# Kernel tuning notes

Measured on AMD Instinct MI355X. Metric: run time of the kernel, lower is better.

Reference implementation:

```python
import jax, jax.numpy as jnp
import numpy as np

B, D_IN, N_NODES, NNZ = 128, 64, 50000, 800000


def setup_inputs() -> dict:
    key = jax.random.key(0)
    k1, k2, k3, k4, k5 = jax.random.split(key, 5)
    x = jax.random.normal(k1, (B, D_IN), dtype=jnp.float32)
    # weight init ~ uniform(-1/sqrt(out), 1/sqrt(out)) per reset(); scale kept tiny
    stdv = 1.0 / np.sqrt(N_NODES)
    weight = jax.random.uniform(k2, (D_IN, N_NODES), dtype=jnp.float32,
                                minval=-stdv, maxval=stdv)
    adj_rows = jax.random.randint(k3, (NNZ,), 0, N_NODES)
    adj_cols = jax.random.randint(k4, (NNZ,), 0, N_NODES)
    adj_vals = jax.random.normal(k5, (NNZ,), dtype=jnp.float32)
    return {"x": x, "weight": weight, "adj_rows": adj_rows,
            "adj_cols": adj_cols, "adj_vals": adj_vals}


def reference(x, weight, adj_rows, adj_cols, adj_vals):
    # m = x @ W : [B, N]
    m = jnp.dot(x, weight)
    # m @ adj (sparse COO): out[b, c] = sum_e m[b, rows[e]] * vals[e] where cols[e] == c
    gathered = m[:, adj_rows] * adj_vals  # [B, NNZ]
    out = jnp.zeros(m.shape, m.dtype).at[:, adj_cols].add(gathered)
    return out
```

## Files before the change

kernel.cpp:

```cpp
#include <hip/hip_runtime.h>

#define B_    128
#define DIN_  64
#define NN_   50000
#define NNZ_  800000
#define CAP_  64
#define NC_   16

#define GEMM_BLOCKS_   782
#define BUCKET_BLOCKS_ 1563
#define FUSED_BLOCKS_  2345

__device__ __forceinline__ unsigned short f2bf(float f) {
    unsigned int u = __float_as_uint(f);
    u += 0x7FFFu + ((u >> 16) & 1u);
    return (unsigned short)(u >> 16);
}

__global__ __launch_bounds__(512) void fused_gb(const float* __restrict__ x,
                                                const float* __restrict__ W,
                                                unsigned short* __restrict__ m_bf,
                                                const int* __restrict__ rows,
                                                const int* __restrict__ cols,
                                                const float* __restrict__ vals,
                                                int* __restrict__ cnt,
                                                unsigned int* __restrict__ csc) {
    __shared__ float xs_t[DIN_][132];
    const int t = threadIdx.x;
    const int g = blockIdx.x / 3;
    const int r = blockIdx.x % 3;

    if (r != 0) {
        const int bid = 2 * g + (r - 1);
        if (bid >= BUCKET_BLOCKS_) return;
        const int e = bid * 512 + t;
        if (e >= NNZ_) return;
        const int c = cols[e];
        const int pos = atomicAdd(&cnt[c], 1);
        if (pos < CAP_)
            csc[((unsigned int)c << 6) + pos] =
                ((unsigned int)rows[e] << 16) | (unsigned int)f2bf(vals[e]);
        return;
    }

    for (int i = t; i < B_ * DIN_; i += 512)
        xs_t[i & 63][i >> 6] = x[i];
    __syncthreads();

    const int l  = t & 63;
    const int n  = g * 64 + l;
    const int nc = n < NN_ ? n : NN_ - 1;
    const int b0 = (t >> 6) * 16;

    float acc[16];
    #pragma unroll
    for (int j = 0; j < 16; ++j) acc[j] = 0.f;

    const float* Wp = W + nc;
    float wcur[8], wnxt[8];
    #pragma unroll
    for (int q = 0; q < 8; ++q) wcur[q] = Wp[(size_t)q * NN_];

    for (int k = 0; k < DIN_; k += 8) {
        const int kn = k + 8;
        if (kn < DIN_) {
            #pragma unroll
            for (int q = 0; q < 8; ++q) wnxt[q] = Wp[(size_t)(kn + q) * NN_];
        }
        #pragma unroll
        for (int q = 0; q < 8; ++q) {
            const float wv = wcur[q];
            const float4* xp = reinterpret_cast<const float4*>(&xs_t[k + q][b0]);
            const float4 x0 = xp[0], x1 = xp[1], x2 = xp[2], x3 = xp[3];
            acc[0]  += wv * x0.x;  acc[1]  += wv * x0.y;
            acc[2]  += wv * x0.z;  acc[3]  += wv * x0.w;
            acc[4]  += wv * x1.x;  acc[5]  += wv * x1.y;
            acc[6]  += wv * x1.z;  acc[7]  += wv * x1.w;
            acc[8]  += wv * x2.x;  acc[9]  += wv * x2.y;
            acc[10] += wv * x2.z;  acc[11] += wv * x2.w;
            acc[12] += wv * x3.x;  acc[13] += wv * x3.y;
            acc[14] += wv * x3.z;  acc[15] += wv * x3.w;
        }
        #pragma unroll
        for (int q = 0; q < 8; ++q) wcur[q] = wnxt[q];
    }

    if (n < NN_) {
        unsigned int pk[8];
        #pragma unroll
        for (int j = 0; j < 8; ++j)
            pk[j] = (unsigned int)f2bf(acc[2 * j]) |
                    ((unsigned int)f2bf(acc[2 * j + 1]) << 16);
        uint4* op = reinterpret_cast<uint4*>(m_bf + (size_t)n * B_ + b0);
        op[0] = make_uint4(pk[0], pk[1], pk[2], pk[3]);
        op[1] = make_uint4(pk[4], pk[5], pk[6], pk[7]);
    }
}

__global__ __launch_bounds__(256) void gather_k(const unsigned short* __restrict__ m_bf,
                                                const int* __restrict__ cnt,
                                                const unsigned int* __restrict__ csc,
                                                float* __restrict__ out) {
    __shared__ float tile[B_][NC_ + 1];
    const int t    = threadIdx.x;
    const int g    = t >> 6;
    const int lane = t & 63;
    const int c0   = blockIdx.x * NC_;

    #pragma unroll
    for (int cl = 0; cl < 4; ++cl) {
        const int c = c0 + g * 4 + cl;
        const unsigned int* ce = &csc[(unsigned int)c << 6];
        int n = cnt[c]; if (n > CAP_) n = CAP_;

        float acc0 = 0.f, acc1 = 0.f;
        int e = 0;
        for (; e + 7 < n; e += 8) {
            unsigned int p[8], mm[8];
            #pragma unroll
            for (int q = 0; q < 8; ++q) p[q] = ce[e + q];
            #pragma unroll
            for (int q = 0; q < 8; ++q)
                mm[q] = *(const unsigned int*)(m_bf + (((size_t)(p[q] >> 16)) << 7) + (lane << 1));
            #pragma unroll
            for (int q = 0; q < 8; ++q) {
                const float v = __uint_as_float(p[q] << 16);
                acc0 += __uint_as_float(mm[q] << 16)         * v;
                acc1 += __uint_as_float(mm[q] & 0xFFFF0000u) * v;
            }
        }
        for (; e + 3 < n; e += 4) {
            unsigned int p[4], mm[4];
            #pragma unroll
            for (int q = 0; q < 4; ++q) p[q] = ce[e + q];
            #pragma unroll
            for (int q = 0; q < 4; ++q)
                mm[q] = *(const unsigned int*)(m_bf + (((size_t)(p[q] >> 16)) << 7) + (lane << 1));
            #pragma unroll
            for (int q = 0; q < 4; ++q) {
                const float v = __uint_as_float(p[q] << 16);
                acc0 += __uint_as_float(mm[q] << 16)         * v;
                acc1 += __uint_as_float(mm[q] & 0xFFFF0000u) * v;
            }
        }
        for (; e < n; ++e) {
            const unsigned int p = ce[e];
            const unsigned int m = *(const unsigned int*)(m_bf + (((size_t)(p >> 16)) << 7) + (lane << 1));
            const float v = __uint_as_float(p << 16);
            acc0 += __uint_as_float(m << 16)         * v;
            acc1 += __uint_as_float(m & 0xFFFF0000u) * v;
        }
        tile[2 * lane][g * 4 + cl]     = acc0;
        tile[2 * lane + 1][g * 4 + cl] = acc1;
    }
    __syncthreads();

    const int r = t >> 1, h = t & 1;
    const float* tr = &tile[r][h * 8];
    const float4 w0 = make_float4(tr[0], tr[1], tr[2], tr[3]);
    const float4 w1 = make_float4(tr[4], tr[5], tr[6], tr[7]);
    float4* op = reinterpret_cast<float4*>(&out[(size_t)r * NN_ + c0 + h * 8]);
    op[0] = w0;
    op[1] = w1;
}

__global__ __launch_bounds__(256) void scatter_onfly(const float* __restrict__ x,
                                                     const float* __restrict__ W,
                                                     const int* __restrict__ rows,
                                                     const int* __restrict__ cols,
                                                     const float* __restrict__ vals,
                                                     float* __restrict__ out) {
    const unsigned int gid = blockIdx.x * 256u + threadIdx.x;
    const unsigned int e = gid >> 7;
    const unsigned int b = gid & 127u;
    if (e >= NNZ_) return;
    const int   r = rows[e];
    const int   c = cols[e];
    const float v = vals[e];
    float dot = 0.f;
    for (int k = 0; k < DIN_; ++k)
        dot += x[b * DIN_ + k] * W[(size_t)k * NN_ + r];
    atomicAdd(&out[(size_t)b * NN_ + c], dot * v);
}

extern "C" void kernel_launch(void* const* d_in, const int* in_sizes, int n_in,
                              void* d_out, int out_size, void* d_ws, size_t ws_size,
                              hipStream_t stream) {
    const float* x    = (const float*)d_in[0];
    const float* W    = (const float*)d_in[1];
    const int*   rows = (const int*)d_in[2];
    const int*   cols = (const int*)d_in[3];
    const float* vals = (const float*)d_in[4];
    float* out = (float*)d_out;

    const size_t mbf_bytes = (size_t)NN_ * B_ * sizeof(unsigned short);
    const size_t cnt_bytes = (size_t)NN_ * sizeof(int);
    const size_t csc_bytes = (size_t)NN_ * CAP_ * sizeof(unsigned int);
    const size_t need = mbf_bytes + cnt_bytes + csc_bytes;

    const int gather_blocks = NN_ / NC_;

    if (ws_size >= need) {
        char* p = (char*)d_ws;
        unsigned short* m_bf = (unsigned short*)p;  p += mbf_bytes;
        int*            cnt  = (int*)p;             p += cnt_bytes;
        unsigned int*   csc  = (unsigned int*)p;

        hipMemsetAsync(cnt, 0, cnt_bytes, stream);
        fused_gb<<<FUSED_BLOCKS_, 512, 0, stream>>>(x, W, m_bf, rows, cols, vals, cnt, csc);
        gather_k<<<gather_blocks, 256, 0, stream>>>(m_bf, cnt, csc, out);
    } else {
        const int scatter_blocks = (NNZ_ * 128) / 256;
        hipMemsetAsync(out, 0, (size_t)NN_ * B_ * sizeof(float), stream);
        scatter_onfly<<<scatter_blocks, 256, 0, stream>>>(x, W, rows, cols, vals, out);
    }
}
```

Before: 165.6 us.

## Fuse memset, GEMM/bucketing and gather into one cooperative persistent kernel

Replaces the memset plus two-kernel pipeline with a single cooperative kernel. It zeroes the counters, runs GEMM and bucketing on alternating blocks, and performs the gather in grid-stride 32-column tiles, with grid.sync barriers between phases. The aim is to remove launch overhead and the inter-kernel gaps. In exchange it adds two grid-wide barriers and a persistent grid sized by occupancy, which may hide memory latency less well in the latency-bound gather phase. The old multi-kernel path is kept as a fallback if the cooperative launch fails.

```diff
diff --git a/kernel.cpp b/kernel.cpp
--- a/kernel.cpp
+++ b/kernel.cpp
@@ -1,21 +1,173 @@
 #include <hip/hip_runtime.h>
+#include <hip/hip_cooperative_groups.h>
+
+namespace cg = cooperative_groups;
 
 #define B_    128
 #define DIN_  64
 #define NN_   50000
 #define NNZ_  800000
 #define CAP_  64
-#define NC_   16
-
-#define GEMM_BLOCKS_   782
-#define BUCKET_BLOCKS_ 1563
-#define FUSED_BLOCKS_  2345
+
+#define GEMM_TILES_   782
+#define GATHER_TILES_ 1563
 
 __device__ __forceinline__ unsigned short f2bf(float f) {
     unsigned int u = __float_as_uint(f);
     u += 0x7FFFu + ((u >> 16) & 1u);
     return (unsigned short)(u >> 16);
 }
+
+__global__ __launch_bounds__(512) void fused_all(const float* __restrict__ x,
+                                                 const float* __restrict__ W,
+                                                 unsigned short* __restrict__ m_bf,
+                                                 const int* __restrict__ rows,
+                                                 const int* __restrict__ cols,
+                                                 const float* __restrict__ vals,
+                                                 int* __restrict__ cnt,
+                                                 unsigned int* __restrict__ csc,
+                                                 float* __restrict__ out) {
+    __shared__ float smem[DIN_ * 132];
+    cg::grid_group grid = cg::this_grid();
+    const int t   = threadIdx.x;
+    const int blk = blockIdx.x;
+    const int nb  = gridDim.x;
+
+    for (int i = blk * 512 + t; i < NN_; i += nb * 512)
+        cnt[i] = 0;
+    grid.sync();
+
+    if (blk & 1) {
+        const int nbb = nb >> 1;
+        const int idx = blk >> 1;
+        for (int e = idx * 512 + t; e < NNZ_; e += nbb * 512) {
+            const int c = cols[e];
+            const int pos = atomicAdd(&cnt[c], 1);
+            if (pos < CAP_)
+                csc[((unsigned int)c << 6) + pos] =
+                    ((unsigned int)rows[e] << 16) | (unsigned int)f2bf(vals[e]);
+        }
+    } else {
+        float (*xs_t)[132] = reinterpret_cast<float (*)[132]>(smem);
+        for (int i = t; i < B_ * DIN_; i += 512)
+            xs_t[i & 63][i >> 6] = x[i];
+        __syncthreads();
+
+        const int nbg = (nb + 1) >> 1;
+        const int idx = blk >> 1;
+        const int l   = t & 63;
+        const int b0  = (t >> 6) * 16;
+
+        for (int tile = idx; tile < GEMM_TILES_; tile += nbg) {
+            const int n  = tile * 64 + l;
+            const int nc = n < NN_ ? n : NN_ - 1;
+
+            float acc[16];
+            #pragma unroll
+            for (int j = 0; j < 16; ++j) acc[j] = 0.f;
+
+            const float* Wp = W + nc;
+            float wcur[8], wnxt[8];
+            #pragma unroll
+            for (int q = 0; q < 8; ++q) wcur[q] = Wp[(size_t)q * NN_];
+
+            for (int k = 0; k < DIN_; k += 8) {
+                const int kn = k + 8;
+                if (kn < DIN_) {
+                    #pragma unroll
+                    for (int q = 0; q < 8; ++q) wnxt[q] = Wp[(size_t)(kn + q) * NN_];
+                }
+                #pragma unroll
+                for (int q = 0; q < 8; ++q) {
+                    const float wv = wcur[q];
+                    const float4* xp = reinterpret_cast<const float4*>(&xs_t[k + q][b0]);
+                    const float4 x0 = xp[0], x1 = xp[1], x2 = xp[2], x3 = xp[3];
+                    acc[0]  += wv * x0.x;  acc[1]  += wv * x0.y;
+                    acc[2]  += wv * x0.z;  acc[3]  += wv * x0.w;
+                    acc[4]  += wv * x1.x;  acc[5]  += wv * x1.y;
+                    acc[6]  += wv * x1.z;  acc[7]  += wv * x1.w;
+                    acc[8]  += wv * x2.x;  acc[9]  += wv * x2.y;
+                    acc[10] += wv * x2.z;  acc[11] += wv * x2.w;
+                    acc[12] += wv * x3.x;  acc[13] += wv * x3.y;
+                    acc[14] += wv * x3.z;  acc[15] += wv * x3.w;
+                }
+                #pragma unroll
+                for (int q = 0; q < 8; ++q) wcur[q] = wnxt[q];
+            }
+
+            if (n < NN_) {
+                unsigned int pk[8];
+                #pragma unroll
+                for (int j = 0; j < 8; ++j)
+                    pk[j] = (unsigned int)f2bf(acc[2 * j]) |
+                            ((unsigned int)f2bf(acc[2 * j + 1]) << 16);
+                uint4* op = reinterpret_cast<uint4*>(m_bf + (size_t)n * B_ + b0);
+                op[0] = make_uint4(pk[0], pk[1], pk[2], pk[3]);
+                op[1] = make_uint4(pk[4], pk[5], pk[6], pk[7]);
+            }
+        }
+    }
+    grid.sync();
+
+    float (*tile)[33] = reinterpret_cast<float (*)[33]>(smem);
+    const int g2   = t >> 6;
+    const int lane = t & 63;
+
+    for (int tt = blk; tt < GATHER_TILES_; tt += nb) {
+        const int c0 = tt * 32;
+
+        #pragma unroll
+        for (int cl = 0; cl < 4; ++cl) {
+            const int c = c0 + g2 * 4 + cl;
+            float acc0 = 0.f, acc1 = 0.f;
+            if (c < NN_) {
+                const unsigned int* ce = &csc[(unsigned int)c << 6];
+                int n = cnt[c]; if (n > CAP_) n = CAP_;
+                int e = 0;
+                for (; e + 7 < n; e += 8) {
+                    unsigned int p[8], mm[8];
+                    #pragma unroll
+                    for (int q = 0; q < 8; ++q) p[q] = ce[e + q];
+                    #pragma unroll
+                    for (int q = 0; q < 8; ++q)
+                        mm[q] = *(const unsigned int*)(m_bf + (((size_t)(p[q] >> 16)) << 7) + (lane << 1));
+                    #pragma unroll
+                    for (int q = 0; q < 8; ++q) {
+                        const float v = __uint_as_float(p[q] << 16);
+                        acc0 += __uint_as_float(mm[q] << 16)         * v;
+                        acc1 += __uint_as_float(mm[q] & 0xFFFF0000u) * v;
+                    }
+                }
+                for (; e < n; ++e) {
+                    const unsigned int p = ce[e];
+                    const unsigned int m = *(const unsigned int*)(m_bf + (((size_t)(p >> 16)) << 7) + (lane << 1));
+                    const float v = __uint_as_float(p << 16);
+                    acc0 += __uint_as_float(m << 16)         * v;
+                    acc1 += __uint_as_float(m & 0xFFFF0000u) * v;
+                }
+            }
+            tile[2 * lane][g2 * 4 + cl]     = acc0;
+            tile[2 * lane + 1][g2 * 4 + cl] = acc1;
+        }
+        __syncthreads();
+
+        const int r = t >> 2, seg = t & 3;
+        const int cbase = c0 + seg * 8;
+        const float* tr = &tile[r][seg * 8];
+        if (cbase + 7 < NN_) {
+            float4* op = reinterpret_cast<float4*>(&out[(size_t)r * NN_ + cbase]);
+            op[0] = make_float4(tr[0], tr[1], tr[2], tr[3]);
+            op[1] = make_float4(tr[4], tr[5], tr[6], tr[7]);
+        } else {
+            for (int j = 0; j < 8; ++j)
+                if (cbase + j < NN_) out[(size_t)r * NN_ + cbase + j] = tr[j];
+        }
+        __syncthreads();
+    }
+}
+
+#define BUCKET_BLOCKS_ 1563
+#define FUSED_BLOCKS_  2345
 
 __global__ __launch_bounds__(512) void fused_gb(const float* __restrict__ x,
                                                 const float* __restrict__ W,
@@ -101,18 +253,17 @@
                                                 const int* __restrict__ cnt,
                                                 const unsigned int* __restrict__ csc,
                                                 float* __restrict__ out) {
-    __shared__ float tile[B_][NC_ + 1];
+    __shared__ float tile[B_][17];
     const int t    = threadIdx.x;
     const int g    = t >> 6;
     const int lane = t & 63;
-    const int c0   = blockIdx.x * NC_;
+    const int c0   = blockIdx.x * 16;
 
     #pragma unroll
     for (int cl = 0; cl < 4; ++cl) {
         const int c = c0 + g * 4 + cl;
         const unsigned int* ce = &csc[(unsigned int)c << 6];
         int n = cnt[c]; if (n > CAP_) n = CAP_;
-
         float acc0 = 0.f, acc1 = 0.f;
         int e = 0;
         for (; e + 7 < n; e += 8) {
@@ -124,20 +275,6 @@
                 mm[q] = *(const unsigned int*)(m_bf + (((size_t)(p[q] >> 16)) << 7) + (lane << 1));
             #pragma unroll
             for (int q = 0; q < 8; ++q) {
-                const float v = __uint_as_float(p[q] << 16);
-                acc0 += __uint_as_float(mm[q] << 16)         * v;
-                acc1 += __uint_as_float(mm[q] & 0xFFFF0000u) * v;
-            }
-        }
-        for (; e + 3 < n; e += 4) {
-            unsigned int p[4], mm[4];
-            #pragma unroll
-            for (int q = 0; q < 4; ++q) p[q] = ce[e + q];
-            #pragma unroll
-            for (int q = 0; q < 4; ++q)
-                mm[q] = *(const unsigned int*)(m_bf + (((size_t)(p[q] >> 16)) << 7) + (lane << 1));
-            #pragma unroll
-            for (int q = 0; q < 4; ++q) {
                 const float v = __uint_as_float(p[q] << 16);
                 acc0 += __uint_as_float(mm[q] << 16)         * v;
                 acc1 += __uint_as_float(mm[q] & 0xFFFF0000u) * v;
@@ -157,11 +294,9 @@
 
     const int r = t >> 1, h = t & 1;
     const float* tr = &tile[r][h * 8];
-    const float4 w0 = make_float4(tr[0], tr[1], tr[2], tr[3]);
-    const float4 w1 = make_float4(tr[4], tr[5], tr[6], tr[7]);
     float4* op = reinterpret_cast<float4*>(&out[(size_t)r * NN_ + c0 + h * 8]);
-    op[0] = w0;
-    op[1] = w1;
+    op[0] = make_float4(tr[0], tr[1], tr[2], tr[3]);
+    op[1] = make_float4(tr[4], tr[5], tr[6], tr[7]);
 }
 
 __global__ __launch_bounds__(256) void scatter_onfly(const float* __restrict__ x,
@@ -198,17 +333,31 @@
     const size_t csc_bytes = (size_t)NN_ * CAP_ * sizeof(unsigned int);
     const size_t need = mbf_bytes + cnt_bytes + csc_bytes;
 
-    const int gather_blocks = NN_ / NC_;
-
     if (ws_size >= need) {
         char* p = (char*)d_ws;
         unsigned short* m_bf = (unsigned short*)p;  p += mbf_bytes;
         int*            cnt  = (int*)p;             p += cnt_bytes;
         unsigned int*   csc  = (unsigned int*)p;
 
-        hipMemsetAsync(cnt, 0, cnt_bytes, stream);
-        fused_gb<<<FUSED_BLOCKS_, 512, 0, stream>>>(x, W, m_bf, rows, cols, vals, cnt, csc);
-        gather_k<<<gather_blocks, 256, 0, stream>>>(m_bf, cnt, csc, out);
+        int maxb = 0;
+        hipError_t oerr = hipOccupancyMaxActiveBlocksPerMultiprocessor(
+            &maxb, (const void*)fused_all, 512, 0);
+        bool done = false;
+        if (oerr == hipSuccess && maxb > 0) {
+            int grid = maxb * 256;
+            if (grid > GATHER_TILES_) grid = GATHER_TILES_;
+            void* args[] = {(void*)&x, (void*)&W, (void*)&m_bf, (void*)&rows,
+                            (void*)&cols, (void*)&vals, (void*)&cnt, (void*)&csc,
+                            (void*)&out};
+            hipError_t lerr = hipLaunchCooperativeKernel(
+                (const void*)fused_all, dim3(grid), dim3(512), args, 0, stream);
+            done = (lerr == hipSuccess);
+        }
+        if (!done) {
+            hipMemsetAsync(cnt, 0, cnt_bytes, stream);
+            fused_gb<<<FUSED_BLOCKS_, 512, 0, stream>>>(x, W, m_bf, rows, cols, vals, cnt, csc);
+            gather_k<<<NN_ / 16, 256, 0, stream>>>(m_bf, cnt, csc, out);
+        }
     } else {
         const int scatter_blocks = (NNZ_ * 128) / 256;
         hipMemsetAsync(out, 0, (size_t)NN_ * B_ * sizeof(float), stream);
```

Measured after the change: 172.2 us. +4.0%, slower.

## Partition bucketing atomics by XCD column range for L2 locality

Applied to the files above, without the earlier changes.

The fused GEMM/bucketing kernel now maps blocks to XCDs using blockIdx & 7. Each bucketing block scans the whole edge list but only inserts edges whose column falls in its XCD's column slice, so the atomics on cnt and the writes to csc stay within one XCD's L2. The cost is that every bucketing block reads cols for all edges (eight times the index traffic), and the mapping relies on round-robin block-to-XCD dispatch. The 4-wide remainder loop in the gather kernel is also removed.

```diff
diff --git a/kernel.cpp b/kernel.cpp
--- a/kernel.cpp
+++ b/kernel.cpp
@@ -5,11 +5,13 @@
 #define NN_   50000
 #define NNZ_  800000
 #define CAP_  64
-#define NC_   16
-
-#define GEMM_BLOCKS_   782
-#define BUCKET_BLOCKS_ 1563
-#define FUSED_BLOCKS_  2345
+
+#define NXCD_      8
+#define COLS_PER_X 6250
+#define SPX_       293
+#define GEMM_Q_    98
+#define NBB_       195
+#define GEMM_TILES_ 782
 
 __device__ __forceinline__ unsigned short f2bf(float f) {
     unsigned int u = __float_as_uint(f);
@@ -17,38 +19,46 @@
     return (unsigned short)(u >> 16);
 }
 
-__global__ __launch_bounds__(512) void fused_gb(const float* __restrict__ x,
-                                                const float* __restrict__ W,
-                                                unsigned short* __restrict__ m_bf,
-                                                const int* __restrict__ rows,
-                                                const int* __restrict__ cols,
-                                                const float* __restrict__ vals,
-                                                int* __restrict__ cnt,
-                                                unsigned int* __restrict__ csc) {
+__global__ __launch_bounds__(512) void fused_gb2(const float* __restrict__ x,
+                                                 const float* __restrict__ W,
+                                                 unsigned short* __restrict__ m_bf,
+                                                 const int* __restrict__ rows,
+                                                 const int* __restrict__ cols,
+                                                 const float* __restrict__ vals,
+                                                 int* __restrict__ cnt,
+                                                 unsigned int* __restrict__ csc) {
     __shared__ float xs_t[DIN_][132];
-    const int t = threadIdx.x;
-    const int g = blockIdx.x / 3;
-    const int r = blockIdx.x % 3;
-
-    if (r != 0) {
-        const int bid = 2 * g + (r - 1);
-        if (bid >= BUCKET_BLOCKS_) return;
-        const int e = bid * 512 + t;
-        if (e >= NNZ_) return;
-        const int c = cols[e];
-        const int pos = atomicAdd(&cnt[c], 1);
-        if (pos < CAP_)
-            csc[((unsigned int)c << 6) + pos] =
-                ((unsigned int)rows[e] << 16) | (unsigned int)f2bf(vals[e]);
+    const int t    = threadIdx.x;
+    const int xcd  = blockIdx.x & 7;
+    const int s    = blockIdx.x >> 3;
+    const int q    = s / 3;
+    const int m    = s % 3;
+
+    if (m != 0) {
+        const int rank = s - (q + 1);
+        const int c_lo = xcd * COLS_PER_X;
+        const int c_hi = c_lo + COLS_PER_X;
+        for (int e = rank * 512 + t; e < NNZ_; e += NBB_ * 512) {
+            const int c = cols[e];
+            if (c >= c_lo && c < c_hi) {
+                const int pos = atomicAdd(&cnt[c], 1);
+                if (pos < CAP_)
+                    csc[((unsigned int)c << 6) + pos] =
+                        ((unsigned int)rows[e] << 16) | (unsigned int)f2bf(vals[e]);
+            }
+        }
         return;
     }
+
+    const int tile = q * 8 + xcd;
+    if (tile >= GEMM_TILES_) return;
 
     for (int i = t; i < B_ * DIN_; i += 512)
         xs_t[i & 63][i >> 6] = x[i];
     __syncthreads();
 
     const int l  = t & 63;
-    const int n  = g * 64 + l;
+    const int n  = tile * 64 + l;
     const int nc = n < NN_ ? n : NN_ - 1;
     const int b0 = (t >> 6) * 16;
 
@@ -59,18 +69,18 @@
     const float* Wp = W + nc;
     float wcur[8], wnxt[8];
     #pragma unroll
-    for (int q = 0; q < 8; ++q) wcur[q] = Wp[(size_t)q * NN_];
+    for (int q2 = 0; q2 < 8; ++q2) wcur[q2] = Wp[(size_t)q2 * NN_];
 
     for (int k = 0; k < DIN_; k += 8) {
         const int kn = k + 8;
         if (kn < DIN_) {
             #pragma unroll
-            for (int q = 0; q < 8; ++q) wnxt[q] = Wp[(size_t)(kn + q) * NN_];
+            for (int q2 = 0; q2 < 8; ++q2) wnxt[q2] = Wp[(size_t)(kn + q2) * NN_];
         }
         #pragma unroll
-        for (int q = 0; q < 8; ++q) {
-            const float wv = wcur[q];
-            const float4* xp = reinterpret_cast<const float4*>(&xs_t[k + q][b0]);
+        for (int q2 = 0; q2 < 8; ++q2) {
+            const float wv = wcur[q2];
+            const float4* xp = reinterpret_cast<const float4*>(&xs_t[k + q2][b0]);
             const float4 x0 = xp[0], x1 = xp[1], x2 = xp[2], x3 = xp[3];
             acc[0]  += wv * x0.x;  acc[1]  += wv * x0.y;
             acc[2]  += wv * x0.z;  acc[3]  += wv * x0.w;
@@ -82,7 +92,7 @@
             acc[14] += wv * x3.z;  acc[15] += wv * x3.w;
         }
         #pragma unroll
-        for (int q = 0; q < 8; ++q) wcur[q] = wnxt[q];
+        for (int q2 = 0; q2 < 8; ++q2) wcur[q2] = wnxt[q2];
     }
 
     if (n < NN_) {
@@ -101,18 +111,17 @@
                                                 const int* __restrict__ cnt,
                                                 const unsigned int* __restrict__ csc,
                                                 float* __restrict__ out) {
-    __shared__ float tile[B_][NC_ + 1];
+    __shared__ float tile[B_][17];
     const int t    = threadIdx.x;
     const int g    = t >> 6;
     const int lane = t & 63;
-    const int c0   = blockIdx.x * NC_;
+    const int c0   = blockIdx.x * 16;
 
     #pragma unroll
     for (int cl = 0; cl < 4; ++cl) {
         const int c = c0 + g * 4 + cl;
         const unsigned int* ce = &csc[(unsigned int)c << 6];
         int n = cnt[c]; if (n > CAP_) n = CAP_;
-
         float acc0 = 0.f, acc1 = 0.f;
         int e = 0;
         for (; e + 7 < n; e += 8) {
@@ -124,20 +133,6 @@
                 mm[q] = *(const unsigned int*)(m_bf + (((size_t)(p[q] >> 16)) << 7) + (lane << 1));
             #pragma unroll
             for (int q = 0; q < 8; ++q) {
-                const float v = __uint_as_float(p[q] << 16);
-                acc0 += __uint_as_float(mm[q] << 16)         * v;
-                acc1 += __uint_as_float(mm[q] & 0xFFFF0000u) * v;
-            }
-        }
-        for (; e + 3 < n; e += 4) {
-            unsigned int p[4], mm[4];
-            #pragma unroll
-            for (int q = 0; q < 4; ++q) p[q] = ce[e + q];
-            #pragma unroll
-            for (int q = 0; q < 4; ++q)
-                mm[q] = *(const unsigned int*)(m_bf + (((size_t)(p[q] >> 16)) << 7) + (lane << 1));
-            #pragma unroll
-            for (int q = 0; q < 4; ++q) {
                 const float v = __uint_as_float(p[q] << 16);
                 acc0 += __uint_as_float(mm[q] << 16)         * v;
                 acc1 += __uint_as_float(mm[q] & 0xFFFF0000u) * v;
@@ -157,11 +152,9 @@
 
     const int r = t >> 1, h = t & 1;
     const float* tr = &tile[r][h * 8];
-    const float4 w0 = make_float4(tr[0], tr[1], tr[2], tr[3]);
-    const float4 w1 = make_float4(tr[4], tr[5], tr[6], tr[7]);
     float4* op = reinterpret_cast<float4*>(&out[(size_t)r * NN_ + c0 + h * 8]);
-    op[0] = w0;
-    op[1] = w1;
+    op[0] = make_float4(tr[0], tr[1], tr[2], tr[3]);
+    op[1] = make_float4(tr[4], tr[5], tr[6], tr[7]);
 }
 
 __global__ __launch_bounds__(256) void scatter_onfly(const float* __restrict__ x,
@@ -198,8 +191,6 @@
     const size_t csc_bytes = (size_t)NN_ * CAP_ * sizeof(unsigned int);
     const size_t need = mbf_bytes + cnt_bytes + csc_bytes;
 
-    const int gather_blocks = NN_ / NC_;
-
     if (ws_size >= need) {
         char* p = (char*)d_ws;
         unsigned short* m_bf = (unsigned short*)p;  p += mbf_bytes;
@@ -207,8 +198,8 @@
         unsigned int*   csc  = (unsigned int*)p;
 
         hipMemsetAsync(cnt, 0, cnt_bytes, stream);
-        fused_gb<<<FUSED_BLOCKS_, 512, 0, stream>>>(x, W, m_bf, rows, cols, vals, cnt, csc);
-        gather_k<<<gather_blocks, 256, 0, stream>>>(m_bf, cnt, csc, out);
+        fused_gb2<<<SPX_ * NXCD_, 512, 0, stream>>>(x, W, m_bf, rows, cols, vals, cnt, csc);
+        gather_k<<<NN_ / 16, 256, 0, stream>>>(m_bf, cnt, csc, out);
     } else {
         const int scatter_blocks = (NNZ_ * 128) / 256;
         hipMemsetAsync(out, 0, (size_t)NN_ * B_ * sizeof(float), stream);
```

Result: slower. 173.1 us (+4.5%).

## Split bf16 intermediate into four batch quarters so each gather pass fits in L2

Applied to the files above, without the earlier changes.

The GEMM output is stored as four batch-quarter slabs of 32 columns each, [4][N][32], in place of row-major [N][128]. The gather kernel now loops over the quarters, so each pass randomly reads only a 3.2MB slab that can stay resident in L2. Each block handles 64 output columns, with two columns per wave split into 32-lane halves. In exchange, every block re-reads the CSC entries and counts four times, each gather loads a 2-byte element instead of 4, and the loop adds extra syncthreads and divergent-length loops.

```diff
diff --git a/kernel.cpp b/kernel.cpp
--- a/kernel.cpp
+++ b/kernel.cpp
@@ -5,11 +5,11 @@
 #define NN_   50000
 #define NNZ_  800000
 #define CAP_  64
-#define NC_   16
-
-#define GEMM_BLOCKS_   782
+
 #define BUCKET_BLOCKS_ 1563
 #define FUSED_BLOCKS_  2345
+#define GEMM_TILES_    782
+#define GQ_BLOCKS_     782
 
 __device__ __forceinline__ unsigned short f2bf(float f) {
     unsigned int u = __float_as_uint(f);
@@ -19,7 +19,7 @@
 
 __global__ __launch_bounds__(512) void fused_gb(const float* __restrict__ x,
                                                 const float* __restrict__ W,
-                                                unsigned short* __restrict__ m_bf,
+                                                unsigned short* __restrict__ m_q,
                                                 const int* __restrict__ rows,
                                                 const int* __restrict__ cols,
                                                 const float* __restrict__ vals,
@@ -86,82 +86,75 @@
     }
 
     if (n < NN_) {
+        const int qq  = b0 >> 5;
+        const int off = b0 & 31;
         unsigned int pk[8];
         #pragma unroll
         for (int j = 0; j < 8; ++j)
             pk[j] = (unsigned int)f2bf(acc[2 * j]) |
                     ((unsigned int)f2bf(acc[2 * j + 1]) << 16);
-        uint4* op = reinterpret_cast<uint4*>(m_bf + (size_t)n * B_ + b0);
+        uint4* op = reinterpret_cast<uint4*>(m_q + ((size_t)qq * NN_ + n) * 32 + off);
         op[0] = make_uint4(pk[0], pk[1], pk[2], pk[3]);
         op[1] = make_uint4(pk[4], pk[5], pk[6], pk[7]);
     }
 }
 
-__global__ __launch_bounds__(256) void gather_k(const unsigned short* __restrict__ m_bf,
-                                                const int* __restrict__ cnt,
-                                                const unsigned int* __restrict__ csc,
-                                                float* __restrict__ out) {
-    __shared__ float tile[B_][NC_ + 1];
+__global__ __launch_bounds__(256) void gather_l2(const unsigned short* __restrict__ m_q,
+                                                 const int* __restrict__ cnt,
+                                                 const unsigned int* __restrict__ csc,
+                                                 float* __restrict__ out) {
+    __shared__ float tile[32][65];
     const int t    = threadIdx.x;
-    const int g    = t >> 6;
+    const int grp  = t >> 6;
     const int lane = t & 63;
-    const int c0   = blockIdx.x * NC_;
-
-    #pragma unroll
-    for (int cl = 0; cl < 4; ++cl) {
-        const int c = c0 + g * 4 + cl;
-        const unsigned int* ce = &csc[(unsigned int)c << 6];
-        int n = cnt[c]; if (n > CAP_) n = CAP_;
-
-        float acc0 = 0.f, acc1 = 0.f;
-        int e = 0;
-        for (; e + 7 < n; e += 8) {
-            unsigned int p[8], mm[8];
-            #pragma unroll
-            for (int q = 0; q < 8; ++q) p[q] = ce[e + q];
-            #pragma unroll
-            for (int q = 0; q < 8; ++q)
-                mm[q] = *(const unsigned int*)(m_bf + (((size_t)(p[q] >> 16)) << 7) + (lane << 1));
-            #pragma unroll
-            for (int q = 0; q < 8; ++q) {
-                const float v = __uint_as_float(p[q] << 16);
-                acc0 += __uint_as_float(mm[q] << 16)         * v;
-                acc1 += __uint_as_float(mm[q] & 0xFFFF0000u) * v;
+    const int half = lane >> 5;
+    const int bl   = lane & 31;
+    const int c0   = blockIdx.x * 64;
+
+    for (int q = 0; q < 4; ++q) {
+        const unsigned short* mbase = m_q + (size_t)q * NN_ * 32;
+
+        for (int s = 0; s < 8; ++s) {
+            const int c = c0 + s * 8 + grp * 2 + half;
+            float acc = 0.f;
+            int n = 0;
+            const unsigned int* ce = csc;
+            if (c < NN_) {
+                n = cnt[c]; if (n > CAP_) n = CAP_;
+                ce = csc + ((unsigned int)c << 6);
             }
-        }
-        for (; e + 3 < n; e += 4) {
-            unsigned int p[4], mm[4];
-            #pragma unroll
-            for (int q = 0; q < 4; ++q) p[q] = ce[e + q];
-            #pragma unroll
-            for (int q = 0; q < 4; ++q)
-                mm[q] = *(const unsigned int*)(m_bf + (((size_t)(p[q] >> 16)) << 7) + (lane << 1));
-            #pragma unroll
-            for (int q = 0; q < 4; ++q) {
-                const float v = __uint_as_float(p[q] << 16);
-                acc0 += __uint_as_float(mm[q] << 16)         * v;
-                acc1 += __uint_as_float(mm[q] & 0xFFFF0000u) * v;
+            for (int i = 0; __any(i < n); i += 8) {
+                unsigned int  p[8];
+                unsigned short mv[8];
+                #pragma unroll
+                for (int j = 0; j < 8; ++j)
+                    p[j] = (i + j < n) ? ce[i + j] : 0u;
+                #pragma unroll
+                for (int j = 0; j < 8; ++j)
+                    mv[j] = mbase[(size_t)(p[j] >> 16) * 32 + bl];
+                #pragma unroll
+                for (int j = 0; j < 8; ++j)
+                    acc += __uint_as_float((unsigned int)mv[j] << 16) *
+                           __uint_as_float(p[j] << 16);
             }
-        }
-        for (; e < n; ++e) {
-            const unsigned int p = ce[e];
-            const unsigned int m = *(const unsigned int*)(m_bf + (((size_t)(p >> 16)) << 7) + (lane << 1));
-            const float v = __uint_as_float(p << 16);
-            acc0 += __uint_as_float(m << 16)         * v;
-            acc1 += __uint_as_float(m & 0xFFFF0000u) * v;
-        }
-        tile[2 * lane][g * 4 + cl]     = acc0;
-        tile[2 * lane + 1][g * 4 + cl] = acc1;
-    }
-    __syncthreads();
-
-    const int r = t >> 1, h = t & 1;
-    const float* tr = &tile[r][h * 8];
-    const float4 w0 = make_float4(tr[0], tr[1], tr[2], tr[3]);
-    const float4 w1 = make_float4(tr[4], tr[5], tr[6], tr[7]);
-    float4* op = reinterpret_cast<float4*>(&out[(size_t)r * NN_ + c0 + h * 8]);
-    op[0] = w0;
-    op[1] = w1;
+            tile[bl][s * 8 + grp * 2 + half] = acc;
+        }
+        __syncthreads();
+
+        const int r = t >> 3, seg = t & 7;
+        const int cbase = c0 + seg * 8;
+        const float* tr = &tile[r][seg * 8];
+        float* orow = &out[(size_t)(q * 32 + r) * NN_];
+        if (cbase + 7 < NN_) {
+            float4* op = reinterpret_cast<float4*>(orow + cbase);
+            op[0] = make_float4(tr[0], tr[1], tr[2], tr[3]);
+            op[1] = make_float4(tr[4], tr[5], tr[6], tr[7]);
+        } else {
+            for (int j = 0; j < 8; ++j)
+                if (cbase + j < NN_) orow[cbase + j] = tr[j];
+        }
+        __syncthreads();
+    }
 }
 
 __global__ __launch_bounds__(256) void scatter_onfly(const float* __restrict__ x,
@@ -198,17 +191,15 @@
     const size_t csc_bytes = (size_t)NN_ * CAP_ * sizeof(unsigned int);
     const size_t need = mbf_bytes + cnt_bytes + csc_bytes;
 
-    const int gather_blocks = NN_ / NC_;
-
     if (ws_size >= need) {
         char* p = (char*)d_ws;
-        unsigned short* m_bf = (unsigned short*)p;  p += mbf_bytes;
-        int*            cnt  = (int*)p;             p += cnt_bytes;
-        unsigned int*   csc  = (unsigned int*)p;
+        unsigned short* m_q = (unsigned short*)p;  p += mbf_bytes;
+        int*            cnt = (int*)p;             p += cnt_bytes;
+        unsigned int*   csc = (unsigned int*)p;
 
         hipMemsetAsync(cnt, 0, cnt_bytes, stream);
-        fused_gb<<<FUSED_BLOCKS_, 512, 0, stream>>>(x, W, m_bf, rows, cols, vals, cnt, csc);
-        gather_k<<<gather_blocks, 256, 0, stream>>>(m_bf, cnt, csc, out);
+        fused_gb <<<FUSED_BLOCKS_, 512, 0, stream>>>(x, W, m_q, rows, cols, vals, cnt, csc);
+        gather_l2<<<GQ_BLOCKS_,    256, 0, stream>>>(m_q, cnt, csc, out);
     } else {
         const int scatter_blocks = (NNZ_ * 128) / 256;
         hipMemsetAsync(out, 0, (size_t)NN_ * B_ * sizeof(float), stream);
```

Result: slower. 223.7 us (+35.1%).
